# Performance work log

Measured on AMD Instinct MI355X. Metric: run time of the kernel, lower is better.

## Reference

```python
import jax, jax.numpy as jnp
import numpy as np

D, H, KV, HD, F = 2048, 16, 4, 128, 5632
WIN, NG = 512, 64          # sliding window size, num global tokens
EPS = 1e-6
KEEP_ATTN = 1.0 - 0.82     # Ramanujan sparsity on attention projections
KEEP_FFN = 1.0 - 0.88      # Ramanujan sparsity on FFN projections


def _mask_w(key, shape, keep):
    """Fixed structured-sparse weight: dense init * binary keep-mask."""
    k1, k2 = jax.random.split(key)
    w = jax.random.normal(k1, shape, dtype=jnp.float32) * (shape[0] ** -0.5)
    m = (jax.random.uniform(k2, shape) < keep).astype(jnp.float32)
    return w * m


def setup_inputs() -> dict:
    key = jax.random.key(0)
    ks = jax.random.split(key, 8)
    x = jax.random.normal(ks[0], (1, 2048, D), dtype=jnp.float32)
    return {
        "x": x,
        "g_attn": jnp.ones((D,), jnp.float32),   # RMSNorm weight (attn)
        "g_ffn": jnp.ones((D,), jnp.float32),    # RMSNorm weight (ffn)
        "wq": _mask_w(ks[1], (D, H * HD), KEEP_ATTN),
        "wk": _mask_w(ks[2], (D, KV * HD), KEEP_ATTN),
        "wv": _mask_w(ks[3], (D, KV * HD), KEEP_ATTN),
        "wo": _mask_w(ks[4], (H * HD, D), KEEP_ATTN),
        "w1": _mask_w(ks[5], (D, F), KEEP_FFN),   # SwiGLU gate proj
        "w3": _mask_w(ks[6], (D, F), KEEP_FFN),   # SwiGLU up proj
        "w2": _mask_w(ks[7], (F, D), KEEP_FFN),   # SwiGLU down proj
    }


def _rmsnorm(x, g):
    return x * jax.lax.rsqrt(jnp.mean(x * x, axis=-1, keepdims=True) + EPS) * g


def _qknorm(t):  # RMS-normalize over head_dim (QK-Normalization)
    return t * jax.lax.rsqrt(jnp.mean(t * t, axis=-1, keepdims=True) + EPS)


def reference(x, g_attn, g_ffn, wq, wk, wv, wo, w1, w2, w3):
    B, S, _ = x.shape
    # --- attention sub-block: x = x + SlidingWindowGQA(RMSNorm(x)) ---
    h = _rmsnorm(x, g_attn)
    q = h @ wq
    q = q.reshape(B, S, H, HD)
    k = (h @ wk).reshape(B, S, KV, HD)
    v = (h @ wv).reshape(B, S, KV, HD)
    q, k = _qknorm(q), _qknorm(k)
    rep = H // KV
    k = jnp.repeat(k, rep, axis=2)  # [B,S,H,HD]
    v = jnp.repeat(v, rep, axis=2)
    scores = jnp.einsum("bihd,bjhd->bhij", q, k) * (HD ** -0.5)
    # causal + (sliding window OR global row OR global column)
    i = jnp.arange(S)[:, None]
    j = jnp.arange(S)[None, :]
    allowed = (j <= i) & (((i - j) < WIN) | (j < NG) | (i < NG))
    scores = jnp.where(allowed[None, None], scores, jnp.float32(-1e30))
    attn = jax.nn.softmax(scores, axis=-1)
    o = jnp.einsum("bhij,bjhd->bihd", attn, v).reshape(B, S, H * HD)
    x = x + o @ wo
    # --- FFN sub-block: x = x + SparseSwiGLU(RMSNorm(x)) ---
    h2 = _rmsnorm(x, g_ffn)
    ffn = (jax.nn.silu(h2 @ w1) * (h2 @ w3)) @ w2
    return x + ffn
```

## Files before the change

kernel.cpp:

```cpp
#include <hip/hip_runtime.h>
#include <hip/hip_bf16.h>
#include <stdint.h>

typedef _Float16 fp16_t;
typedef __attribute__((ext_vector_type(8))) _Float16 fp16x8;
typedef __attribute__((ext_vector_type(4))) _Float16 fp16x4;
typedef __attribute__((ext_vector_type(2))) _Float16 fp16x2;
typedef __attribute__((ext_vector_type(4))) float f32x4;

#define WIN 512
#define NG 64

__device__ __forceinline__ void gload16(const void* g, void* l) {
    __builtin_amdgcn_global_load_lds((const __attribute__((address_space(1))) void*)g,
                                     (__attribute__((address_space(3))) void*)l, 16, 0, 0);
}

__device__ __forceinline__ void wait_vm8() { asm volatile("s_waitcnt vmcnt(8)" ::: "memory"); }
__device__ __forceinline__ void wait_vm6() { asm volatile("s_waitcnt vmcnt(6)" ::: "memory"); }
__device__ __forceinline__ void wait_vm0() { asm volatile("s_waitcnt vmcnt(0)" ::: "memory"); }

__device__ __forceinline__ void tr_tile(const float* __restrict__ src, int C, int srow, int scol,
                                        fp16_t* __restrict__ out, int R, int orow) {
    __shared__ fp16_t t[64][66];
    int tid = threadIdx.x;
    int tx = tid & 15, ty = tid >> 4;
#pragma unroll
    for (int j = 0; j < 4; ++j) {
        int r = ty + j * 16;
        float4 v = *(const float4*)&src[(size_t)(srow + r) * C + scol + tx * 4];
        fp16x2 a = { (fp16_t)v.x, (fp16_t)v.y };
        fp16x2 b = { (fp16_t)v.z, (fp16_t)v.w };
        *(fp16x2*)&t[r][tx * 4] = a;
        *(fp16x2*)&t[r][tx * 4 + 2] = b;
    }
    __syncthreads();
#pragma unroll
    for (int jj = 0; jj < 4; ++jj) {
        int c = ty + jj * 16;
        fp16x4 o = { t[tx * 4 + 0][c], t[tx * 4 + 1][c], t[tx * 4 + 2][c], t[tx * 4 + 3][c] };
        *(fp16x4*)&out[(size_t)(orow + c) * R + srow + tx * 4] = o;
    }
}

__global__ __launch_bounds__(256) void transpose_qkv3(const float* __restrict__ wq,
                                                      const float* __restrict__ wk,
                                                      const float* __restrict__ wv,
                                                      fp16_t* __restrict__ out) {
    int n0 = blockIdx.x * 64, k0 = blockIdx.y * 64;
    const float* src; int C, c0;
    if (n0 < 2048)      { src = wq; C = 2048; c0 = n0; }
    else if (n0 < 2560) { src = wk; C = 512;  c0 = n0 - 2048; }
    else                { src = wv; C = 512;  c0 = n0 - 2560; }
    tr_tile(src, C, k0, c0, out, 2048, n0);
}

__global__ __launch_bounds__(256) void transpose_w13(const float* __restrict__ w1,
                                                     const float* __restrict__ w3,
                                                     fp16_t* __restrict__ o1,
                                                     fp16_t* __restrict__ o3) {
    const float* src = blockIdx.z ? w3 : w1;
    fp16_t* out = blockIdx.z ? o3 : o1;
    tr_tile(src, 5632, blockIdx.y * 64, blockIdx.x * 64, out, 2048, blockIdx.x * 64);
}

__global__ __launch_bounds__(256) void transpose_one(const float* __restrict__ src,
                                                     fp16_t* __restrict__ out, int R, int C) {
    tr_tile(src, C, blockIdx.y * 64, blockIdx.x * 64, out, R, blockIdx.x * 64);
}

__global__ __launch_bounds__(256) void rmsnorm_kernel(const float* __restrict__ in,
                                                      const float* __restrict__ g,
                                                      fp16_t* __restrict__ out) {
    int row = blockIdx.x;
    int tid = threadIdx.x;
    const float4* rp = (const float4*)(in + (size_t)row * 2048);
    float4 v0 = rp[tid], v1 = rp[tid + 256];
    float ss = v0.x * v0.x + v0.y * v0.y + v0.z * v0.z + v0.w * v0.w +
               v1.x * v1.x + v1.y * v1.y + v1.z * v1.z + v1.w * v1.w;
#pragma unroll
    for (int m = 1; m < 64; m <<= 1) ss += __shfl_xor(ss, m);
    __shared__ float red[4];
    if ((tid & 63) == 0) red[tid >> 6] = ss;
    __syncthreads();
    ss = red[0] + red[1] + red[2] + red[3];
    float sc = rsqrtf(ss * (1.0f / 2048.0f) + 1e-6f);
    const float4* gp = (const float4*)g;
    float4 g0 = gp[tid], g1 = gp[tid + 256];
    fp16x4 o0 = { (fp16_t)(v0.x * sc * g0.x), (fp16_t)(v0.y * sc * g0.y),
                  (fp16_t)(v0.z * sc * g0.z), (fp16_t)(v0.w * sc * g0.w) };
    fp16x4 o1 = { (fp16_t)(v1.x * sc * g1.x), (fp16_t)(v1.y * sc * g1.y),
                  (fp16_t)(v1.z * sc * g1.z), (fp16_t)(v1.w * sc * g1.w) };
    *(fp16x4*)(out + (size_t)row * 2048 + tid * 4) = o0;
    *(fp16x4*)(out + (size_t)row * 2048 + 1024 + tid * 4) = o1;
}

#define BM 128
#define BN 128
#define BKK 64

struct GemmCore {
    int tid, lane, wid, lo, hi, wr, wc;
    int arow[4], ascb[4];
    __device__ __forceinline__ void init(int t) {
        tid = t; lane = t & 63; wid = t >> 6;
        lo = lane & 15; hi = lane >> 4;
        wr = (wid >> 1) * 64; wc = (wid & 1) * 64;
#pragma unroll
        for (int p = 0; p < 4; ++p) {
            int idx = (wid * 4 + p) * 64 + lane;
            int row = idx >> 3;
            int cb = (idx & 7) << 4;
            arow[p] = row;
            ascb[p] = cb ^ ((row & 7) << 4);
        }
    }
    __device__ __forceinline__ void stage(char* buf, const fp16_t* A, const fp16_t* Bt,
                                          int brow, int bcol, int lda, int ldb, int kb) {
        char* As = buf;
        char* Bs = buf + 16384;
#pragma unroll
        for (int p = 0; p < 4; ++p) {
            int ci = wid * 4 + p;
            gload16((const char*)A + ((size_t)(brow + arow[p]) * lda + kb) * 2 + ascb[p],
                    As + ci * 1024);
            gload16((const char*)Bt + ((size_t)(bcol + arow[p]) * ldb + kb) * 2 + ascb[p],
                    Bs + ci * 1024);
        }
    }
    __device__ __forceinline__ void compute(const char* buf, f32x4 (&acc)[4][4]) {
        const char* As = buf;
        const char* Bs = buf + 16384;
#pragma unroll
        for (int kc = 0; kc < 2; ++kc) {
            fp16x8 af[4], bfr[4];
            int boff = kc * 64 + hi * 16;
#pragma unroll
            for (int m = 0; m < 4; ++m) {
                int row = wr + m * 16 + lo;
                af[m] = *(const fp16x8*)(As + row * 128 + (boff ^ ((row & 7) << 4)));
            }
#pragma unroll
            for (int n = 0; n < 4; ++n) {
                int row = wc + n * 16 + lo;
                bfr[n] = *(const fp16x8*)(Bs + row * 128 + (boff ^ ((row & 7) << 4)));
            }
#pragma unroll
            for (int m = 0; m < 4; ++m)
#pragma unroll
                for (int n = 0; n < 4; ++n)
                    acc[m][n] = __builtin_amdgcn_mfma_f32_16x16x32_f16(af[m], bfr[n], acc[m][n], 0, 0, 0);
        }
    }
};

__global__ __launch_bounds__(256, 2) void gemm_qkv(const fp16_t* __restrict__ A,
                                                   const fp16_t* __restrict__ Bt,
                                                   fp16_t* __restrict__ Cout,
                                                   fp16_t* __restrict__ vT,
                                                   int M, int N, int K) {
    __shared__ __align__(16) char smem[2][32768];
    GemmCore g;
    g.init(threadIdx.x);
    int brow = blockIdx.y * BM, bcol = blockIdx.x * BN;
    int nK = K / BKK;

    f32x4 acc[4][4] = {};
    g.stage(smem[0], A, Bt, brow, bcol, K, K, 0);
    for (int kt = 0; kt < nK; ++kt) {
        if (kt + 1 < nK) {
            g.stage(smem[(kt + 1) & 1], A, Bt, brow, bcol, K, K, (kt + 1) * BKK);
            wait_vm8();
        } else {
            wait_vm0();
        }
        __builtin_amdgcn_s_barrier();
        __builtin_amdgcn_sched_barrier(0);
        g.compute(smem[kt & 1], acc);
        __builtin_amdgcn_s_barrier();
    }

    if (blockIdx.x < 20) {
        float* sq = (float*)smem;
        bool isq = blockIdx.x < 16;
#pragma unroll
        for (int m = 0; m < 4; ++m)
#pragma unroll
            for (int r = 0; r < 4; ++r) {
                float s = 0.f;
#pragma unroll
                for (int n = 0; n < 4; ++n) s += acc[m][n][r] * acc[m][n][r];
                s += __shfl_xor(s, 1); s += __shfl_xor(s, 2);
                s += __shfl_xor(s, 4); s += __shfl_xor(s, 8);
                if (g.lo == 0) sq[g.wid * 64 + m * 16 + g.hi * 4 + r] = s;
            }
        __syncthreads();
#pragma unroll
        for (int m = 0; m < 4; ++m)
#pragma unroll
            for (int r = 0; r < 4; ++r) {
                int rl = m * 16 + g.hi * 4 + r;
                float tot = sq[g.wid * 64 + rl] + sq[(g.wid ^ 1) * 64 + rl];
                float sc = rsqrtf(tot * (1.0f / 128.0f) + 1e-6f);
                if (isq) sc *= 0.08838834764831843f;
#pragma unroll
                for (int n = 0; n < 4; ++n) acc[m][n][r] *= sc;
            }
#pragma unroll
        for (int m = 0; m < 4; ++m) {
            int grow0 = brow + g.wr + m * 16 + g.hi * 4;
#pragma unroll
            for (int n = 0; n < 4; ++n) {
                int gcol = bcol + g.wc + n * 16 + g.lo;
#pragma unroll
                for (int r = 0; r < 4; ++r)
                    Cout[(size_t)(grow0 + r) * N + gcol] = (fp16_t)acc[m][n][r];
            }
        }
    } else {
#pragma unroll
        for (int m = 0; m < 4; ++m) {
            int gcol0 = brow + g.wr + m * 16 + g.hi * 4;
#pragma unroll
            for (int n = 0; n < 4; ++n) {
                int vrow = bcol + g.wc + n * 16 + g.lo - 2560;
                fp16x4 o = { (fp16_t)acc[m][n][0], (fp16_t)acc[m][n][1],
                             (fp16_t)acc[m][n][2], (fp16_t)acc[m][n][3] };
                *(fp16x4*)&vT[(size_t)vrow * 2048 + gcol0] = o;
            }
        }
    }
}

__global__ __launch_bounds__(256, 2) void gemm_bt64_resid(const fp16_t* __restrict__ A,
                                                          const fp16_t* __restrict__ Bt,
                                                          float* __restrict__ Cout,
                                                          const float* __restrict__ resid,
                                                          int M, int N, int K) {
    __shared__ __align__(16) char smem[2][24576];
    int tid = threadIdx.x, lane = tid & 63, wid = tid >> 6;
    int lo = lane & 15, hi = lane >> 4;
    int wr = (wid >> 1) * 64, wc = (wid & 1) * 32;
    int brow = blockIdx.y * 128, bcol = blockIdx.x * 64;
    int nK = K / BKK;

    int arow[4], ascb[4];
#pragma unroll
    for (int p = 0; p < 4; ++p) {
        int idx = (wid * 4 + p) * 64 + lane;
        int row = idx >> 3;
        int cb = (idx & 7) << 4;
        arow[p] = row;
        ascb[p] = cb ^ ((row & 7) << 4);
    }
    int brow_[2], bscb[2];
#pragma unroll
    for (int p = 0; p < 2; ++p) {
        int idx = (wid * 2 + p) * 64 + lane;
        int row = idx >> 3;
        int cb = (idx & 7) << 4;
        brow_[p] = row;
        bscb[p] = cb ^ ((row & 7) << 4);
    }

    auto stage = [&](char* buf, int kb) {
        char* As = buf;
        char* Bs = buf + 16384;
#pragma unroll
        for (int p = 0; p < 4; ++p)
            gload16((const char*)A + ((size_t)(brow + arow[p]) * K + kb) * 2 + ascb[p],
                    As + (wid * 4 + p) * 1024);
#pragma unroll
        for (int p = 0; p < 2; ++p)
            gload16((const char*)Bt + ((size_t)(bcol + brow_[p]) * K + kb) * 2 + bscb[p],
                    Bs + (wid * 2 + p) * 1024);
    };

    f32x4 acc[4][2] = {};
    stage(smem[0], 0);
    for (int kt = 0; kt < nK; ++kt) {
        if (kt + 1 < nK) {
            stage(smem[(kt + 1) & 1], (kt + 1) * BKK);
            wait_vm6();
        } else {
            wait_vm0();
        }
        __builtin_amdgcn_s_barrier();
        __builtin_amdgcn_sched_barrier(0);
        const char* As = smem[kt & 1];
        const char* Bs = As + 16384;
#pragma unroll
        for (int kc = 0; kc < 2; ++kc) {
            fp16x8 af[4], bfr[2];
            int boff = kc * 64 + hi * 16;
#pragma unroll
            for (int m = 0; m < 4; ++m) {
                int row = wr + m * 16 + lo;
                af[m] = *(const fp16x8*)(As + row * 128 + (boff ^ ((row & 7) << 4)));
            }
#pragma unroll
            for (int n = 0; n < 2; ++n) {
                int row = wc + n * 16 + lo;
                bfr[n] = *(const fp16x8*)(Bs + row * 128 + (boff ^ ((row & 7) << 4)));
            }
#pragma unroll
            for (int m = 0; m < 4; ++m)
#pragma unroll
                for (int n = 0; n < 2; ++n)
                    acc[m][n] = __builtin_amdgcn_mfma_f32_16x16x32_f16(af[m], bfr[n], acc[m][n], 0, 0, 0);
        }
        __builtin_amdgcn_s_barrier();
    }

#pragma unroll
    for (int m = 0; m < 4; ++m) {
        int grow0 = brow + wr + m * 16 + hi * 4;
#pragma unroll
        for (int n = 0; n < 2; ++n) {
            int gcol = bcol + wc + n * 16 + lo;
#pragma unroll
            for (int r = 0; r < 4; ++r) {
                size_t gidx = (size_t)(grow0 + r) * N + gcol;
                Cout[gidx] = acc[m][n][r] + resid[gidx];
            }
        }
    }
}

__global__ __launch_bounds__(256, 2) void gemm_u1u3_half(const fp16_t* __restrict__ A,
                                                         const fp16_t* __restrict__ Bt1,
                                                         const fp16_t* __restrict__ Bt3,
                                                         fp16_t* __restrict__ G,
                                                         int M, int N, int K) {
    __shared__ __align__(16) char smem[2][32768];
    int tid = threadIdx.x, lane = tid & 63, wid = tid >> 6;
    int lo = lane & 15, hi = lane >> 4;
    int wr = (wid >> 1) * 64, wc = (wid & 1) * 32;
    int brow = blockIdx.y * 128, bcol = blockIdx.x * 64;
    int nK = K / BKK;

    int arow[4], ascb[4];
#pragma unroll
    for (int p = 0; p < 4; ++p) {
        int idx = (wid * 4 + p) * 64 + lane;
        int row = idx >> 3;
        int cb = (idx & 7) << 4;
        arow[p] = row;
        ascb[p] = cb ^ ((row & 7) << 4);
    }
    int brow_[2], bscb[2];
#pragma unroll
    for (int p = 0; p < 2; ++p) {
        int idx = (wid * 2 + p) * 64 + lane;
        int row = idx >> 3;
        int cb = (idx & 7) << 4;
        brow_[p] = row;
        bscb[p] = cb ^ ((row & 7) << 4);
    }

    auto stage = [&](char* buf, int kb) {
        char* As = buf;
        char* B1s = buf + 16384;
        char* B3s = buf + 24576;
#pragma unroll
        for (int p = 0; p < 4; ++p)
            gload16((const char*)A + ((size_t)(brow + arow[p]) * K + kb) * 2 + ascb[p],
                    As + (wid * 4 + p) * 1024);
#pragma unroll
        for (int p = 0; p < 2; ++p) {
            gload16((const char*)Bt1 + ((size_t)(bcol + brow_[p]) * K + kb) * 2 + bscb[p],
                    B1s + (wid * 2 + p) * 1024);
            gload16((const char*)Bt3 + ((size_t)(bcol + brow_[p]) * K + kb) * 2 + bscb[p],
                    B3s + (wid * 2 + p) * 1024);
        }
    };

    f32x4 acc1[4][2] = {}, acc3[4][2] = {};
    stage(smem[0], 0);
    for (int kt = 0; kt < nK; ++kt) {
        if (kt + 1 < nK) {
            stage(smem[(kt + 1) & 1], (kt + 1) * BKK);
            wait_vm8();
        } else {
            wait_vm0();
        }
        __builtin_amdgcn_s_barrier();
        __builtin_amdgcn_sched_barrier(0);
        const char* As = smem[kt & 1];
        const char* B1s = As + 16384;
        const char* B3s = As + 24576;
#pragma unroll
        for (int kc = 0; kc < 2; ++kc) {
            fp16x8 af[4], b1f[2], b3f[2];
            int boff = kc * 64 + hi * 16;
#pragma unroll
            for (int m = 0; m < 4; ++m) {
                int row = wr + m * 16 + lo;
                af[m] = *(const fp16x8*)(As + row * 128 + (boff ^ ((row & 7) << 4)));
            }
#pragma unroll
            for (int n = 0; n < 2; ++n) {
                int row = wc + n * 16 + lo;
                int o = row * 128 + (boff ^ ((row & 7) << 4));
                b1f[n] = *(const fp16x8*)(B1s + o);
                b3f[n] = *(const fp16x8*)(B3s + o);
            }
#pragma unroll
            for (int m = 0; m < 4; ++m)
#pragma unroll
                for (int n = 0; n < 2; ++n) {
                    acc1[m][n] = __builtin_amdgcn_mfma_f32_16x16x32_f16(af[m], b1f[n], acc1[m][n], 0, 0, 0);
                    acc3[m][n] = __builtin_amdgcn_mfma_f32_16x16x32_f16(af[m], b3f[n], acc3[m][n], 0, 0, 0);
                }
        }
        __builtin_amdgcn_s_barrier();
    }

#pragma unroll
    for (int m = 0; m < 4; ++m) {
        int grow0 = brow + wr + m * 16 + hi * 4;
#pragma unroll
        for (int n = 0; n < 2; ++n) {
            int gcol = bcol + wc + n * 16 + lo;
#pragma unroll
            for (int r = 0; r < 4; ++r) {
                float u = acc1[m][n][r];
                float val = (u / (1.0f + __expf(-u))) * acc3[m][n][r];
                G[(size_t)(grow0 + r) * N + gcol] = (fp16_t)val;
            }
        }
    }
}

__global__ __launch_bounds__(256, 2) void attn_kernel(const fp16_t* __restrict__ qkv,
                                                      const fp16_t* __restrict__ vT,
                                                      fp16_t* __restrict__ o) {
    __shared__ __align__(16) char smem[16384 + 16384 + 4 * 2304];
    char* Ks = smem;
    char* VTs = smem + 16384;
    char* Ps = smem + 32768;

    int t = blockIdx.x, qh = blockIdx.y;
    int kvh = qh >> 2;
    int qs = t * 64;
    int tid = threadIdx.x, lane = tid & 63, wid = tid >> 6;
    int lo = lane & 15, hi = lane >> 4;

    fp16x8 qf[4];
    {
        const fp16_t* qptr = qkv + (size_t)(qs + wid * 16 + lo) * 3072 + qh * 128 + hi * 8;
#pragma unroll
        for (int kc = 0; kc < 4; ++kc) qf[kc] = *(const fp16x8*)(qptr + kc * 32);
    }

    f32x4 oacc[8] = {};
    float m_r[4], l_r[4];
#pragma unroll
    for (int r = 0; r < 4; ++r) { m_r[r] = -1e30f; l_r[r] = 0.0f; }

    int lot = qs - (WIN - 1);
    int jt_lo = lot <= 0 ? 0 : (lot >> 6);
    int nt = (jt_lo > 0) ? (t - jt_lo + 2) : (t + 1);

    for (int ti = 0; ti < nt; ++ti) {
        int jt = (jt_lo > 0) ? (ti == 0 ? 0 : jt_lo + ti - 1) : ti;
        int js = jt * 64;
        __syncthreads();
#pragma unroll
        for (int p = 0; p < 4; ++p) {
            int ci = wid * 4 + p;
            int idx = ci * 64 + lane;
            int krow = idx >> 4;
            int kcb = (idx & 15) << 4;
            int kscb = kcb ^ ((krow & 7) << 4);
            gload16((const char*)qkv + ((size_t)(js + krow) * 3072 + 2048 + kvh * 128) * 2 + kscb,
                    Ks + ci * 1024);
            int vrow = idx >> 3;
            int vcb = (idx & 7) << 4;
            int vscb = vcb ^ ((vrow & 7) << 4);
            gload16((const char*)vT + ((size_t)(kvh * 128 + vrow) * 2048 + js) * 2 + vscb,
                    VTs + ci * 1024);
        }
        __syncthreads();

        f32x4 s[4] = {};
#pragma unroll
        for (int kc = 0; kc < 4; ++kc) {
#pragma unroll
            for (int jc = 0; jc < 4; ++jc) {
                int row = jc * 16 + lo;
                fp16x8 kf = *(const fp16x8*)(Ks + row * 256 + ((kc * 64 + hi * 16) ^ ((row & 7) << 4)));
                s[jc] = __builtin_amdgcn_mfma_f32_16x16x32_f16(qf[kc], kf, s[jc], 0, 0, 0);
            }
        }

        float mt[4] = { -1e30f, -1e30f, -1e30f, -1e30f };
#pragma unroll
        for (int jc = 0; jc < 4; ++jc) {
            int j = js + jc * 16 + lo;
#pragma unroll
            for (int r = 0; r < 4; ++r) {
                int i = qs + wid * 16 + hi * 4 + r;
                bool ok = (j <= i) && (((i - j) < WIN) || (j < NG) || (i < NG));
                float sv = ok ? s[jc][r] : -1e30f;
                s[jc][r] = sv;
                mt[r] = fmaxf(mt[r], sv);
            }
        }
#pragma unroll
        for (int m2 = 1; m2 <= 8; m2 <<= 1)
#pragma unroll
            for (int r = 0; r < 4; ++r) mt[r] = fmaxf(mt[r], __shfl_xor(mt[r], m2));
        float sf[4], psum[4];
#pragma unroll
        for (int r = 0; r < 4; ++r) {
            float mn = fmaxf(m_r[r], mt[r]);
            sf[r] = __expf(m_r[r] - mn);
            m_r[r] = mn;
            psum[r] = 0.0f;
        }
#pragma unroll
        for (int jc = 0; jc < 4; ++jc)
#pragma unroll
            for (int r = 0; r < 4; ++r) {
                float p = __expf(s[jc][r] - m_r[r]);
                s[jc][r] = p;
                psum[r] += p;
            }
#pragma unroll
        for (int m2 = 1; m2 <= 8; m2 <<= 1)
#pragma unroll
            for (int r = 0; r < 4; ++r) psum[r] += __shfl_xor(psum[r], m2);
#pragma unroll
        for (int r = 0; r < 4; ++r) l_r[r] = l_r[r] * sf[r] + psum[r];
#pragma unroll
        for (int nc = 0; nc < 8; ++nc)
#pragma unroll
            for (int r = 0; r < 4; ++r) oacc[nc][r] *= sf[r];

        char* Pb = Ps + wid * 2304;
#pragma unroll
        for (int jc = 0; jc < 4; ++jc)
#pragma unroll
            for (int r = 0; r < 4; ++r)
                *(fp16_t*)(Pb + (hi * 4 + r) * 144 + (jc * 16 + lo) * 2) = (fp16_t)s[jc][r];
        fp16x8 pa[2];
#pragma unroll
        for (int jc2 = 0; jc2 < 2; ++jc2)
            pa[jc2] = *(const fp16x8*)(Pb + lo * 144 + jc2 * 64 + hi * 16);

#pragma unroll
        for (int jc2 = 0; jc2 < 2; ++jc2)
#pragma unroll
            for (int nc = 0; nc < 8; ++nc) {
                int row = nc * 16 + lo;
                fp16x8 vf = *(const fp16x8*)(VTs + row * 128 + ((jc2 * 64 + hi * 16) ^ ((row & 7) << 4)));
                oacc[nc] = __builtin_amdgcn_mfma_f32_16x16x32_f16(pa[jc2], vf, oacc[nc], 0, 0, 0);
            }
    }

#pragma unroll
    for (int r = 0; r < 4; ++r) {
        float inv = 1.0f / l_r[r];
        int orow = qs + wid * 16 + hi * 4 + r;
#pragma unroll
        for (int nc = 0; nc < 8; ++nc)
            o[(size_t)orow * 2048 + qh * 128 + nc * 16 + lo] = (fp16_t)(oacc[nc][r] * inv);
    }
}

extern "C" void kernel_launch(void* const* d_in, const int* in_sizes, int n_in,
                              void* d_out, int out_size, void* d_ws, size_t ws_size,
                              hipStream_t stream) {
    const float* x = (const float*)d_in[0];
    const float* g_attn = (const float*)d_in[1];
    const float* g_ffn = (const float*)d_in[2];
    const float* wq = (const float*)d_in[3];
    const float* wk = (const float*)d_in[4];
    const float* wv = (const float*)d_in[5];
    const float* wo = (const float*)d_in[6];
    const float* w1 = (const float*)d_in[7];
    const float* w3 = (const float*)d_in[8];
    const float* w2 = (const float*)d_in[9];
    float* out = (float*)d_out;

    char* ws = (char*)d_ws;
    size_t off = 0;
    auto alloc = [&](size_t bytes) {
        char* p = ws + off;
        off += (bytes + 255) & ~(size_t)255;
        return p;
    };
    fp16_t* hbuf  = (fp16_t*)alloc(2048ull * 2048 * 2);
    fp16_t* wqkvT = (fp16_t*)alloc(3072ull * 2048 * 2);
    fp16_t* vTb   = (fp16_t*)alloc(512ull * 2048 * 2);
    fp16_t* qkv   = (fp16_t*)alloc(2048ull * 3072 * 2);
    fp16_t* gbuf  = (fp16_t*)alloc(2048ull * 5632 * 2);
    fp16_t* wbigT = (fp16_t*)alloc(5632ull * 2048 * 2);
    if (off > ws_size) {
        hipMemsetAsync(d_out, 0, (size_t)out_size * 4, stream);
        return;
    }
    fp16_t* w3T = hbuf;

    transpose_qkv3<<<dim3(48, 32), 256, 0, stream>>>(wq, wk, wv, wqkvT);
    rmsnorm_kernel<<<2048, 256, 0, stream>>>(x, g_attn, hbuf);
    gemm_qkv<<<dim3(24, 16), 256, 0, stream>>>(hbuf, wqkvT, qkv, vTb, 2048, 3072, 2048);
    attn_kernel<<<dim3(32, 16), 256, 0, stream>>>(qkv, vTb, hbuf);
    transpose_one<<<dim3(32, 32), 256, 0, stream>>>(wo, wqkvT, 2048, 2048);
    gemm_bt64_resid<<<dim3(32, 16), 256, 0, stream>>>(hbuf, wqkvT, out, x, 2048, 2048, 2048);
    rmsnorm_kernel<<<2048, 256, 0, stream>>>(out, g_ffn, qkv);
    transpose_w13<<<dim3(88, 32, 2), 256, 0, stream>>>(w1, w3, wbigT, w3T);
    gemm_u1u3_half<<<dim3(88, 16), 256, 0, stream>>>(qkv, wbigT, w3T, gbuf, 2048, 5632, 2048);
    transpose_one<<<dim3(32, 88), 256, 0, stream>>>(w2, wbigT, 5632, 2048);
    gemm_bt64_resid<<<dim3(32, 16), 256, 0, stream>>>(gbuf, wbigT, out, out, 2048, 2048, 5632);
}
```

Before: 295.3 us.

## Double-buffer K/V tiles in attention kernel and skip masking on full tiles

The attention kernel now holds two LDS buffers for K and V^T and issues the async global-to-LDS loads for the next key tile before computing on the current one, waiting with vmcnt so load latency overlaps MFMA work. It also skips the per-element causal/window mask evaluation on tiles that are known to be fully allowed, and raises wave priority around the MFMA loops. This doubles LDS use to about 74KB per block, which may reduce how many blocks fit per CU. The 'full' tile test and the barrier placement must exactly match the mask semantics.

```diff
diff --git a/kernel.cpp b/kernel.cpp
--- a/kernel.cpp
+++ b/kernel.cpp
@@ -435,10 +435,8 @@
 __global__ __launch_bounds__(256, 2) void attn_kernel(const fp16_t* __restrict__ qkv,
                                                       const fp16_t* __restrict__ vT,
                                                       fp16_t* __restrict__ o) {
-    __shared__ __align__(16) char smem[16384 + 16384 + 4 * 2304];
-    char* Ks = smem;
-    char* VTs = smem + 16384;
-    char* Ps = smem + 32768;
+    __shared__ __align__(16) char smem[2 * 32768 + 4 * 2304];
+    char* Ps = smem + 65536;
 
     int t = blockIdx.x, qh = blockIdx.y;
     int kvh = qh >> 2;
@@ -462,14 +460,14 @@
     int jt_lo = lot <= 0 ? 0 : (lot >> 6);
     int nt = (jt_lo > 0) ? (t - jt_lo + 2) : (t + 1);
 
-    for (int ti = 0; ti < nt; ++ti) {
-        int jt = (jt_lo > 0) ? (ti == 0 ? 0 : jt_lo + ti - 1) : ti;
-        int js = jt * 64;
-        __syncthreads();
+    int kci = wid * 4, idxb = lane;
+    auto stagekv = [&](char* buf, int js) {
+        char* Ks = buf;
+        char* VTs = buf + 16384;
 #pragma unroll
         for (int p = 0; p < 4; ++p) {
-            int ci = wid * 4 + p;
-            int idx = ci * 64 + lane;
+            int ci = kci + p;
+            int idx = ci * 64 + idxb;
             int krow = idx >> 4;
             int kcb = (idx & 15) << 4;
             int kscb = kcb ^ ((krow & 7) << 4);
@@ -481,9 +479,28 @@
             gload16((const char*)vT + ((size_t)(kvh * 128 + vrow) * 2048 + js) * 2 + vscb,
                     VTs + ci * 1024);
         }
-        __syncthreads();
+    };
+    auto jt_of = [&](int ti) { return (jt_lo > 0) ? (ti == 0 ? 0 : jt_lo + ti - 1) : ti; };
+
+    stagekv(smem, jt_of(0) * 64);
+
+    for (int ti = 0; ti < nt; ++ti) {
+        if (ti + 1 < nt) {
+            stagekv(smem + ((ti + 1) & 1) * 32768, jt_of(ti + 1) * 64);
+            wait_vm8();
+        } else {
+            wait_vm0();
+        }
+        __builtin_amdgcn_s_barrier();
+        __builtin_amdgcn_sched_barrier(0);
+
+        char* Ks = smem + (ti & 1) * 32768;
+        char* VTs = Ks + 16384;
+        int jt = jt_of(ti);
+        int js = jt * 64;
 
         f32x4 s[4] = {};
+        __builtin_amdgcn_s_setprio(1);
 #pragma unroll
         for (int kc = 0; kc < 4; ++kc) {
 #pragma unroll
@@ -493,18 +510,27 @@
                 s[jc] = __builtin_amdgcn_mfma_f32_16x16x32_f16(qf[kc], kf, s[jc], 0, 0, 0);
             }
         }
+        __builtin_amdgcn_s_setprio(0);
 
         float mt[4] = { -1e30f, -1e30f, -1e30f, -1e30f };
-#pragma unroll
-        for (int jc = 0; jc < 4; ++jc) {
-            int j = js + jc * 16 + lo;
-#pragma unroll
-            for (int r = 0; r < 4; ++r) {
-                int i = qs + wid * 16 + hi * 4 + r;
-                bool ok = (j <= i) && (((i - j) < WIN) || (j < NG) || (i < NG));
-                float sv = ok ? s[jc][r] : -1e30f;
-                s[jc][r] = sv;
-                mt[r] = fmaxf(mt[r], sv);
+        bool full = (jt < t) && !((t >= 9) && (jt == t - 8));
+        if (full) {
+#pragma unroll
+            for (int jc = 0; jc < 4; ++jc)
+#pragma unroll
+                for (int r = 0; r < 4; ++r) mt[r] = fmaxf(mt[r], s[jc][r]);
+        } else {
+#pragma unroll
+            for (int jc = 0; jc < 4; ++jc) {
+                int j = js + jc * 16 + lo;
+#pragma unroll
+                for (int r = 0; r < 4; ++r) {
+                    int i = qs + wid * 16 + hi * 4 + r;
+                    bool ok = (j <= i) && (((i - j) < WIN) || (j < NG) || (i < NG));
+                    float sv = ok ? s[jc][r] : -1e30f;
+                    s[jc][r] = sv;
+                    mt[r] = fmaxf(mt[r], sv);
+                }
             }
         }
 #pragma unroll
@@ -549,6 +575,7 @@
         for (int jc2 = 0; jc2 < 2; ++jc2)
             pa[jc2] = *(const fp16x8*)(Pb + lo * 144 + jc2 * 64 + hi * 16);
 
+        __builtin_amdgcn_s_setprio(1);
 #pragma unroll
         for (int jc2 = 0; jc2 < 2; ++jc2)
 #pragma unroll
@@ -557,6 +584,9 @@
                 fp16x8 vf = *(const fp16x8*)(VTs + row * 128 + ((jc2 * 64 + hi * 16) ^ ((row & 7) << 4)));
                 oacc[nc] = __builtin_amdgcn_mfma_f32_16x16x32_f16(pa[jc2], vf, oacc[nc], 0, 0, 0);
             }
+        __builtin_amdgcn_s_setprio(0);
+
+        __builtin_amdgcn_s_barrier();
     }
 
 #pragma unroll
```

Result: no change. 297.1 us (+0.6%).
